# Kernel optimization log

Hardware: AMD Instinct MI355X
Metric: run time of the kernel (lower is better)

## Reference

```python
import jax, jax.numpy as jnp
import numpy as np

D_MODEL, D_STATE, B, S = 1024, 64, 8, 2048


def setup_inputs() -> dict:
    key = jax.random.key(0)
    ks = jax.random.split(key, 14)
    inp = {"x": jax.random.normal(ks[0], (B, S, D_MODEL), jnp.float32)}
    names = ["cog", "beh", "env", "delta", "Bp", "Cp"]
    for i, n in enumerate(names):
        inp[f"W_{n}"] = jax.random.normal(ks[1 + 2 * i], (D_STATE, D_MODEL), jnp.float32) / np.sqrt(D_MODEL)
        inp[f"b_{n}"] = jnp.zeros((D_STATE,), jnp.float32)
    # torch init is log(|randn|+1e-4); we use strictly-negative A_log so the
    # length-2048 multiplicative recurrence stays finite (A_log is a learned
    # parameter, so its value is free; the math of forward is unchanged).
    inp["A_log"] = -jnp.abs(jax.random.normal(ks[13], (D_STATE, D_STATE), jnp.float32)) - 0.1
    return inp


def reference(x, W_cog, b_cog, W_beh, b_beh, W_env, b_env,
              W_delta, b_delta, W_Bp, b_Bp, W_Cp, b_Cp, A_log):
    # gating terms (computed in the source but never used downstream)
    A_t = (jax.nn.sigmoid(x @ W_cog.T + b_cog)
           * jax.nn.sigmoid(x @ W_beh.T + b_beh)
           * jax.nn.sigmoid(x @ W_env.T + b_env))
    del A_t

    delta = jax.nn.softplus(x @ W_delta.T + b_delta)   # [B,S,N]
    Bt = x @ W_Bp.T + b_Bp                             # [B,S,N]
    Ct = x @ W_Cp.T + b_Cp                             # [B,S,N]
    u = Bt * x[:, :, :D_STATE]                         # [B,S,N]

    # Faithful to torch broadcasting: after step 0 the carried state h is
    # [B,N,N] with h[b,i,j] = exp(A_log[i,j]*delta[b,t,i]) * h_prev[b,i,j] + u[b,t,j]
    def step(h, td):
        d, u_t, c_t = td                               # each [B,N]
        A = jnp.exp(A_log[None, :, :] * d[:, :, None]) # [B,N,N]
        h = A * h + u_t[:, None, :]
        y = jnp.einsum('bj,bij->bi', c_t, h)           # [B,N]
        return h, y

    h0 = jnp.zeros((x.shape[0], D_STATE, D_STATE), x.dtype)
    _, ys = jax.lax.scan(
        step, h0,
        (delta.transpose(1, 0, 2), u.transpose(1, 0, 2), Ct.transpose(1, 0, 2)))
    # torch stacks y_t of shape [B,1,N] along dim=1 -> [B,S,1,N]
    return ys.transpose(1, 0, 2)[:, :, None, :]
```

## Files before the change

kernel.cpp:

```cpp
#include <hip/hip_runtime.h>
#include <math.h>

#define DM   1024
#define DS   64
#define BATCH 8
#define SEQ  2048
#define CL   32
#define NC   64

typedef __bf16 bf16x8 __attribute__((ext_vector_type(8)));
typedef float  f32x4  __attribute__((ext_vector_type(4)));

#if __has_builtin(__builtin_amdgcn_exp2f)
#define EXP2(v) __builtin_amdgcn_exp2f(v)
#else
#define EXP2(v) __expf(0.69314718056f * (v))
#endif

__global__ __launch_bounds__(256) void wconv_kernel(
    const float* __restrict__ Wd, const float* __restrict__ Wb,
    const float* __restrict__ Wc, __bf16* __restrict__ Wp)
{
    int idx = blockIdx.x * 256 + threadIdx.x;
    int k  = idx & 1023;
    int n  = idx >> 10;
    const float* W = (n < 64) ? Wd : (n < 128 ? Wb : Wc);
    float v = W[(size_t)(n & 63) * DM + k];
    int kt = k >> 5, kk = k & 31;
    Wp[((size_t)kt * 192 + n) * 32 + kk] = (__bf16)v;
}

__global__ __launch_bounds__(512, 2) void projp1_full(
    const float* __restrict__ x, const __bf16* __restrict__ Wp,
    const float* __restrict__ bd, const float* __restrict__ bb,
    const float* __restrict__ bc, const float* __restrict__ A_log,
    float* __restrict__ delta_g, float* __restrict__ u_g,
    float* __restrict__ ct_g,
    float* __restrict__ E, float* __restrict__ Dsum)
{
    __shared__ __bf16 sA[4][64 * 72];
    __shared__ float  s_d[2][CL * 64];
    __shared__ float  s_u[2][CL * 64];

    const int tid  = threadIdx.x;
    const int row0 = blockIdx.x * 64;

    const int lane = tid & 63, wv = tid >> 6;
    const int l15  = lane & 15, quad = lane >> 4;
    const int cw   = wv & 3;
    const int rh   = wv >> 2;
    const int nbase = cw * 48;
    const int rbase = rh * 32;

    const int am = tid >> 3;
    const int ak = tid & 7;
    const float* xga = x + (size_t)(row0 + am) * DM + ak * 8;

    const __bf16* wpb = Wp + (nbase + l15) * 32 + quad * 8;

    f32x4 acc[2][3];
    #pragma unroll
    for (int mt = 0; mt < 2; ++mt)
        #pragma unroll
        for (int nt = 0; nt < 3; ++nt)
            acc[mt][nt] = (f32x4){0.f, 0.f, 0.f, 0.f};

    float4 areg[4];
    bf16x8 bA[6], bB[6];

    #define LOADA2(pp) do {                                                   \
        areg[0] = *(const float4*)(xga + (pp) * 128);                         \
        areg[1] = *(const float4*)(xga + (pp) * 128 + 4);                     \
        areg[2] = *(const float4*)(xga + (pp) * 128 + 64);                    \
        areg[3] = *(const float4*)(xga + (pp) * 128 + 68);                    \
    } while (0)
    #define STAGEA2(be, bo) do {                                              \
        bf16x8 h0 = {(__bf16)areg[0].x, (__bf16)areg[0].y,                    \
                     (__bf16)areg[0].z, (__bf16)areg[0].w,                    \
                     (__bf16)areg[1].x, (__bf16)areg[1].y,                    \
                     (__bf16)areg[1].z, (__bf16)areg[1].w};                   \
        *(bf16x8*)&sA[be][am * 72 + ak * 8] = h0;                             \
        bf16x8 h1 = {(__bf16)areg[2].x, (__bf16)areg[2].y,                    \
                     (__bf16)areg[2].z, (__bf16)areg[2].w,                    \
                     (__bf16)areg[3].x, (__bf16)areg[3].y,                    \
                     (__bf16)areg[3].z, (__bf16)areg[3].w};                   \
        *(bf16x8*)&sA[bo][am * 72 + ak * 8] = h1;                             \
    } while (0)
    #define LOADBF(dst, kb) do {                                              \
        const __bf16* wb_ = wpb + (size_t)(kb) * 12288;                       \
        dst[0] = *(const bf16x8*)(wb_);                                       \
        dst[1] = *(const bf16x8*)(wb_ + 512);                                 \
        dst[2] = *(const bf16x8*)(wb_ + 1024);                                \
        dst[3] = *(const bf16x8*)(wb_ + 6144);                                \
        dst[4] = *(const bf16x8*)(wb_ + 6656);                                \
        dst[5] = *(const bf16x8*)(wb_ + 7168);                                \
    } while (0)
    #define COMPUTE(bi, bfr) do {                                             \
        _Pragma("unroll")                                                     \
        for (int s = 0; s < 2; ++s) {                                         \
            bf16x8 af0 = *(const bf16x8*)                                     \
                &sA[bi][(rbase + l15) * 72 + s * 32 + quad * 8];              \
            bf16x8 af1 = *(const bf16x8*)                                     \
                &sA[bi][(rbase + 16 + l15) * 72 + s * 32 + quad * 8];         \
            _Pragma("unroll")                                                 \
            for (int nt = 0; nt < 3; ++nt) {                                  \
                acc[0][nt] = __builtin_amdgcn_mfma_f32_16x16x32_bf16(         \
                    af0, bfr[s * 3 + nt], acc[0][nt], 0, 0, 0);               \
                acc[1][nt] = __builtin_amdgcn_mfma_f32_16x16x32_bf16(         \
                    af1, bfr[s * 3 + nt], acc[1][nt], 0, 0, 0);               \
            }                                                                 \
        }                                                                     \
    } while (0)

    LOADA2(0);
    STAGEA2(0, 1);
    LOADA2(1);
    LOADBF(bA, 0);
    __syncthreads();

    for (int p = 0; p < 8; ++p) {
        const int pe = (p & 1) * 2, po = pe + 1;
        LOADBF(bB, 2 * p + 1);
        COMPUTE(pe, bA);
        if (p < 7) STAGEA2(pe ^ 2, po ^ 2);
        if (p < 6) LOADA2(p + 2);
        if (p < 7) LOADBF(bA, 2 * p + 2);
        COMPUTE(po, bB);
        __syncthreads();
    }
    #undef LOADA2
    #undef STAGEA2
    #undef LOADBF
    #undef COMPUTE

    #pragma unroll
    for (int nt = 0; nt < 3; ++nt) {
        int gn  = nbase + nt * 16 + l15;
        int mat = (nbase + nt * 16) >> 6;
        int col = gn & 63;
        float bias = (mat == 0) ? bd[col] : (mat == 1 ? bb[col] : bc[col]);
        #pragma unroll
        for (int mt = 0; mt < 2; ++mt) {
            #pragma unroll
            for (int r = 0; r < 4; ++r) {
                int tl = mt * 16 + quad * 4 + r;
                int m  = row0 + rbase + tl;
                float v = acc[mt][nt][r] + bias;
                if (mat == 0) {
                    float sp = (v > 20.f) ? v : __logf(1.f + __expf(v));
                    delta_g[(size_t)m * DS + col] = sp;
                    s_d[rh][tl * 64 + col] = sp;
                } else if (mat == 1) {
                    float uu = v * x[(size_t)m * DM + col];
                    u_g[(size_t)m * DS + col] = uu;
                    s_u[rh][tl * 64 + col] = uu;
                } else {
                    ct_g[(size_t)m * DS + col] = v;
                }
            }
        }
    }
    __syncthreads();

    const int half = tid >> 8;
    const int bidx = blockIdx.x >> 5;
    const int cidx = (blockIdx.x * 2 + half) & 63;
    const int si = tid & 63;
    const int sj = (tid >> 6) & 3;

    float alog[16];
    {
        const float4* ar = (const float4*)(A_log + si * 64 + sj * 16);
        #pragma unroll
        for (int qq = 0; qq < 4; ++qq) {
            float4 v = ar[qq];
            alog[4*qq+0] = v.x * 1.44269504f; alog[4*qq+1] = v.y * 1.44269504f;
            alog[4*qq+2] = v.z * 1.44269504f; alog[4*qq+3] = v.w * 1.44269504f;
        }
    }

    float h[16];
    #pragma unroll
    for (int k = 0; k < 16; ++k) h[k] = 0.f;
    float dsum = 0.f;

    for (int t = 0; t < CL; ++t) {
        float d = s_d[half][t * 64 + si];
        dsum += d;
        const float* up = s_u[half] + t * 64 + sj * 16;
        #pragma unroll
        for (int k = 0; k < 16; ++k)
            h[k] = EXP2(alog[k] * d) * h[k] + up[k];
    }

    float* eo = E + (((size_t)cidx * BATCH + bidx) * 64 + si) * 64 + sj * 16;
    #pragma unroll
    for (int qq = 0; qq < 4; ++qq)
        ((float4*)eo)[qq] = make_float4(h[4*qq], h[4*qq+1], h[4*qq+2], h[4*qq+3]);
    if (sj == 0) Dsum[((size_t)cidx * BATCH + bidx) * 64 + si] = dsum;
}

__device__ __forceinline__ void scan_range8(
    const float* __restrict__ Eb, const float* __restrict__ Db,
    int n0, int n1, int bb_, int i_, int jg_,
    const float* __restrict__ alog, float* __restrict__ h)
{
    if (n0 >= n1) return;
    size_t idx = ((size_t)n0 * BATCH + bb_) * 64 + i_;
    float dsA = Db[idx];
    const float4* ep = (const float4*)(Eb + idx * 64 + jg_ * 8);
    float4 e0 = ep[0], e1 = ep[1];
    for (int n = n0; n < n1; ++n) {
        float dsN = 0.f;
        float4 f0 = make_float4(0.f,0.f,0.f,0.f), f1 = f0;
        if (n + 1 < n1) {
            size_t idx2 = ((size_t)(n + 1) * BATCH + bb_) * 64 + i_;
            dsN = Db[idx2];
            const float4* fp = (const float4*)(Eb + idx2 * 64 + jg_ * 8);
            f0 = fp[0]; f1 = fp[1];
        }
        float ev[8] = {e0.x,e0.y,e0.z,e0.w, e1.x,e1.y,e1.z,e1.w};
        #pragma unroll
        for (int k = 0; k < 8; ++k)
            h[k] = EXP2(alog[k] * dsA) * h[k] + ev[k];
        dsA = dsN; e0 = f0; e1 = f1;
    }
}

__global__ __launch_bounds__(512) void group_kernel(
    const float* __restrict__ E, const float* __restrict__ Dsum,
    const float* __restrict__ A_log,
    float* __restrict__ Eg, float* __restrict__ Dg)
{
    const int g2 = blockIdx.x >> 3, b2 = blockIdx.x & 7;
    const int tid = threadIdx.x;
    const int i  = tid >> 3;
    const int jg = tid & 7;

    float alog[8];
    {
        const float4* ar = (const float4*)(A_log + i * 64 + jg * 8);
        float4 v0 = ar[0], v1 = ar[1];
        alog[0] = v0.x * 1.44269504f; alog[1] = v0.y * 1.44269504f;
        alog[2] = v0.z * 1.44269504f; alog[3] = v0.w * 1.44269504f;
        alog[4] = v1.x * 1.44269504f; alog[5] = v1.y * 1.44269504f;
        alog[6] = v1.z * 1.44269504f; alog[7] = v1.w * 1.44269504f;
    }

    float hg[8];
    #pragma unroll
    for (int k = 0; k < 8; ++k) hg[k] = 0.f;
    scan_range8(E, Dsum, g2 * 8, g2 * 8 + 8, b2, i, jg, alog, hg);

    float4* ego = (float4*)(Eg + (((size_t)g2 * BATCH + b2) * 64 + i) * 64 + jg * 8);
    ego[0] = make_float4(hg[0], hg[1], hg[2], hg[3]);
    ego[1] = make_float4(hg[4], hg[5], hg[6], hg[7]);
    if (jg == 0) {
        float Dacc = 0.f;
        #pragma unroll
        for (int q = 0; q < 8; ++q)
            Dacc += Dsum[((size_t)(g2 * 8 + q) * BATCH + b2) * 64 + i];
        Dg[((size_t)g2 * BATCH + b2) * 64 + i] = Dacc;
    }
}

__global__ __launch_bounds__(512) void pass23_kernel(
    const float* __restrict__ delta_g, const float* __restrict__ u_g,
    const float* __restrict__ ct_g, const float* __restrict__ A_log,
    const float* __restrict__ E, const float* __restrict__ Dsum,
    const float* __restrict__ Eg, const float* __restrict__ Dg,
    float* __restrict__ out)
{
    __shared__ float s_d[CL * 64];
    __shared__ float s_u[CL * 64];
    __shared__ float s_c[CL * 64];

    const int c = blockIdx.x, b = blockIdx.y, tid = threadIdx.x;
    const int t0 = c * CL;

    {
        const float4* dg = (const float4*)(delta_g + ((size_t)b * SEQ + t0) * DS);
        const float4* ug = (const float4*)(u_g     + ((size_t)b * SEQ + t0) * DS);
        const float4* cg = (const float4*)(ct_g    + ((size_t)b * SEQ + t0) * DS);
        ((float4*)s_d)[tid] = dg[tid];
        ((float4*)s_u)[tid] = ug[tid];
        ((float4*)s_c)[tid] = cg[tid];
    }

    const int i  = tid >> 3;
    const int jg = tid & 7;

    float alog[8];
    {
        const float4* ar = (const float4*)(A_log + i * 64 + jg * 8);
        float4 v0 = ar[0], v1 = ar[1];
        alog[0] = v0.x * 1.44269504f; alog[1] = v0.y * 1.44269504f;
        alog[2] = v0.z * 1.44269504f; alog[3] = v0.w * 1.44269504f;
        alog[4] = v1.x * 1.44269504f; alog[5] = v1.y * 1.44269504f;
        alog[6] = v1.z * 1.44269504f; alog[7] = v1.w * 1.44269504f;
    }

    float h[8];
    #pragma unroll
    for (int k = 0; k < 8; ++k) h[k] = 0.f;
    const int g = c >> 3;
    scan_range8(Eg, Dg, 0, g, b, i, jg, alog, h);
    scan_range8(E, Dsum, g * 8, c, b, i, jg, alog, h);
    __syncthreads();

    for (int t = 0; t < CL; ++t) {
        float d = s_d[t * 64 + i];
        const float* up  = s_u + t * 64 + jg * 8;
        const float* cp2 = s_c + t * 64 + jg * 8;
        float part = 0.f;
        #pragma unroll
        for (int k = 0; k < 8; ++k) {
            h[k] = EXP2(alog[k] * d) * h[k] + up[k];
            part += cp2[k] * h[k];
        }
        part += __shfl_xor(part, 1);
        part += __shfl_xor(part, 2);
        part += __shfl_xor(part, 4);
        if (jg == 0)
            out[((size_t)b * SEQ + t0 + t) * DS + i] = part;
    }
}

extern "C" void kernel_launch(void* const* d_in, const int* in_sizes, int n_in,
                              void* d_out, int out_size, void* d_ws, size_t ws_size,
                              hipStream_t stream)
{
    (void)in_sizes; (void)n_in; (void)out_size; (void)ws_size;
    const float* x     = (const float*)d_in[0];
    const float* Wd    = (const float*)d_in[7];
    const float* bd    = (const float*)d_in[8];
    const float* Wb    = (const float*)d_in[9];
    const float* bb    = (const float*)d_in[10];
    const float* Wc    = (const float*)d_in[11];
    const float* bc    = (const float*)d_in[12];
    const float* A_log = (const float*)d_in[13];
    float* out = (float*)d_out;

    float* ws = (float*)d_ws;
    float* delta_g = ws;
    float* u_g     = ws + 1 * 1048576;
    float* ct_g    = ws + 2 * 1048576;
    float* E       = ws + 3 * 1048576;
    float* Dsum    = ws + 5242880;
    float* Eg      = ws + 5275648;
    float* Dg      = ws + 5537792;
    __bf16* Wp     = (__bf16*)(ws + 5541888);

    wconv_kernel<<<768, 256, 0, stream>>>(Wd, Wb, Wc, Wp);
    projp1_full<<<256, 512, 0, stream>>>(
        x, Wp, bd, bb, bc, A_log, delta_g, u_g, ct_g, E, Dsum);
    group_kernel<<<64, 512, 0, stream>>>(E, Dsum, A_log, Eg, Dg);
    pass23_kernel<<<dim3(NC, BATCH), 512, 0, stream>>>(
        delta_g, u_g, ct_g, A_log, E, Dsum, Eg, Dg, out);
}
```

Before: 170.0 us.

## Halve projection block row tile to 32 rows and double the grid

The fused projection plus chunk-scan kernel now processes 32 rows per block instead of 64, launching 512 blocks instead of 256. Each block handles one 32-step chunk, with each thread scanning 8 state columns instead of 16. Launch bounds are raised to 4 blocks per CU. The aim is more parallelism and occupancy across the CUs (256 blocks was roughly one per CU), at the cost of each block reusing the weight fragments over fewer rows and higher register pressure.

```diff
diff --git a/kernel.cpp b/kernel.cpp
--- a/kernel.cpp
+++ b/kernel.cpp
@@ -30,7 +30,7 @@
     Wp[((size_t)kt * 192 + n) * 32 + kk] = (__bf16)v;
 }
 
-__global__ __launch_bounds__(512, 2) void projp1_full(
+__global__ __launch_bounds__(512, 4) void projp1_full(
     const float* __restrict__ x, const __bf16* __restrict__ Wp,
     const float* __restrict__ bd, const float* __restrict__ bb,
     const float* __restrict__ bc, const float* __restrict__ A_log,
@@ -38,53 +38,46 @@
     float* __restrict__ ct_g,
     float* __restrict__ E, float* __restrict__ Dsum)
 {
-    __shared__ __bf16 sA[4][64 * 72];
-    __shared__ float  s_d[2][CL * 64];
-    __shared__ float  s_u[2][CL * 64];
+    __shared__ __bf16 sA[4][32 * 72];
+    __shared__ float  s_d[CL * 64];
+    __shared__ float  s_u[CL * 64];
 
     const int tid  = threadIdx.x;
-    const int row0 = blockIdx.x * 64;
+    const int row0 = blockIdx.x * 32;
 
     const int lane = tid & 63, wv = tid >> 6;
     const int l15  = lane & 15, quad = lane >> 4;
     const int cw   = wv & 3;
     const int rh   = wv >> 2;
     const int nbase = cw * 48;
-    const int rbase = rh * 32;
-
-    const int am = tid >> 3;
-    const int ak = tid & 7;
-    const float* xga = x + (size_t)(row0 + am) * DM + ak * 8;
+    const int rbase = rh * 16;
+
+    const int am    = tid >> 4;
+    const int aslot = tid & 15;
+    const int asub  = aslot >> 3;
+    const int aoff  = (aslot & 7) * 8;
+    const float* xga = x + (size_t)(row0 + am) * DM + aslot * 8;
 
     const __bf16* wpb = Wp + (nbase + l15) * 32 + quad * 8;
 
-    f32x4 acc[2][3];
-    #pragma unroll
-    for (int mt = 0; mt < 2; ++mt)
-        #pragma unroll
-        for (int nt = 0; nt < 3; ++nt)
-            acc[mt][nt] = (f32x4){0.f, 0.f, 0.f, 0.f};
-
-    float4 areg[4];
+    f32x4 acc[3];
+    #pragma unroll
+    for (int nt = 0; nt < 3; ++nt)
+        acc[nt] = (f32x4){0.f, 0.f, 0.f, 0.f};
+
+    float4 areg[2];
     bf16x8 bA[6], bB[6];
 
     #define LOADA2(pp) do {                                                   \
         areg[0] = *(const float4*)(xga + (pp) * 128);                         \
         areg[1] = *(const float4*)(xga + (pp) * 128 + 4);                     \
-        areg[2] = *(const float4*)(xga + (pp) * 128 + 64);                    \
-        areg[3] = *(const float4*)(xga + (pp) * 128 + 68);                    \
     } while (0)
-    #define STAGEA2(be, bo) do {                                              \
-        bf16x8 h0 = {(__bf16)areg[0].x, (__bf16)areg[0].y,                    \
+    #define STAGEA2(be) do {                                                  \
+        bf16x8 hv = {(__bf16)areg[0].x, (__bf16)areg[0].y,                    \
                      (__bf16)areg[0].z, (__bf16)areg[0].w,                    \
                      (__bf16)areg[1].x, (__bf16)areg[1].y,                    \
                      (__bf16)areg[1].z, (__bf16)areg[1].w};                   \
-        *(bf16x8*)&sA[be][am * 72 + ak * 8] = h0;                             \
-        bf16x8 h1 = {(__bf16)areg[2].x, (__bf16)areg[2].y,                    \
-                     (__bf16)areg[2].z, (__bf16)areg[2].w,                    \
-                     (__bf16)areg[3].x, (__bf16)areg[3].y,                    \
-                     (__bf16)areg[3].z, (__bf16)areg[3].w};                   \
-        *(bf16x8*)&sA[bo][am * 72 + ak * 8] = h1;                             \
+        *(bf16x8*)&sA[(be) + asub][am * 72 + aoff] = hv;                      \
     } while (0)
     #define LOADBF(dst, kb) do {                                              \
         const __bf16* wb_ = wpb + (size_t)(kb) * 12288;                       \
@@ -98,22 +91,17 @@
     #define COMPUTE(bi, bfr) do {                                             \
         _Pragma("unroll")                                                     \
         for (int s = 0; s < 2; ++s) {                                         \
-            bf16x8 af0 = *(const bf16x8*)                                     \
+            bf16x8 af = *(const bf16x8*)                                      \
                 &sA[bi][(rbase + l15) * 72 + s * 32 + quad * 8];              \
-            bf16x8 af1 = *(const bf16x8*)                                     \
-                &sA[bi][(rbase + 16 + l15) * 72 + s * 32 + quad * 8];         \
             _Pragma("unroll")                                                 \
-            for (int nt = 0; nt < 3; ++nt) {                                  \
-                acc[0][nt] = __builtin_amdgcn_mfma_f32_16x16x32_bf16(         \
-                    af0, bfr[s * 3 + nt], acc[0][nt], 0, 0, 0);               \
-                acc[1][nt] = __builtin_amdgcn_mfma_f32_16x16x32_bf16(         \
-                    af1, bfr[s * 3 + nt], acc[1][nt], 0, 0, 0);               \
-            }                                                                 \
+            for (int nt = 0; nt < 3; ++nt)                                    \
+                acc[nt] = __builtin_amdgcn_mfma_f32_16x16x32_bf16(            \
+                    af, bfr[s * 3 + nt], acc[nt], 0, 0, 0);                   \
         }                                                                     \
     } while (0)
 
     LOADA2(0);
-    STAGEA2(0, 1);
+    STAGEA2(0);
     LOADA2(1);
     LOADBF(bA, 0);
     __syncthreads();
@@ -122,7 +110,7 @@
         const int pe = (p & 1) * 2, po = pe + 1;
         LOADBF(bB, 2 * p + 1);
         COMPUTE(pe, bA);
-        if (p < 7) STAGEA2(pe ^ 2, po ^ 2);
+        if (p < 7) STAGEA2(pe ^ 2);
         if (p < 6) LOADA2(p + 2);
         if (p < 7) LOADBF(bA, 2 * p + 2);
         COMPUTE(po, bB);
@@ -140,64 +128,58 @@
         int col = gn & 63;
         float bias = (mat == 0) ? bd[col] : (mat == 1 ? bb[col] : bc[col]);
         #pragma unroll
-        for (int mt = 0; mt < 2; ++mt) {
-            #pragma unroll
-            for (int r = 0; r < 4; ++r) {
-                int tl = mt * 16 + quad * 4 + r;
-                int m  = row0 + rbase + tl;
-                float v = acc[mt][nt][r] + bias;
-                if (mat == 0) {
-                    float sp = (v > 20.f) ? v : __logf(1.f + __expf(v));
-                    delta_g[(size_t)m * DS + col] = sp;
-                    s_d[rh][tl * 64 + col] = sp;
-                } else if (mat == 1) {
-                    float uu = v * x[(size_t)m * DM + col];
-                    u_g[(size_t)m * DS + col] = uu;
-                    s_u[rh][tl * 64 + col] = uu;
-                } else {
-                    ct_g[(size_t)m * DS + col] = v;
-                }
+        for (int r = 0; r < 4; ++r) {
+            int tl = rbase + quad * 4 + r;
+            int m  = row0 + tl;
+            float v = acc[nt][r] + bias;
+            if (mat == 0) {
+                float sp = (v > 20.f) ? v : __logf(1.f + __expf(v));
+                delta_g[(size_t)m * DS + col] = sp;
+                s_d[tl * 64 + col] = sp;
+            } else if (mat == 1) {
+                float uu = v * x[(size_t)m * DM + col];
+                u_g[(size_t)m * DS + col] = uu;
+                s_u[tl * 64 + col] = uu;
+            } else {
+                ct_g[(size_t)m * DS + col] = v;
             }
         }
     }
     __syncthreads();
 
-    const int half = tid >> 8;
-    const int bidx = blockIdx.x >> 5;
-    const int cidx = (blockIdx.x * 2 + half) & 63;
-    const int si = tid & 63;
-    const int sj = (tid >> 6) & 3;
-
-    float alog[16];
+    const int bidx = blockIdx.x >> 6;
+    const int cidx = blockIdx.x & 63;
+    const int i  = tid >> 3;
+    const int jg = tid & 7;
+
+    float alog[8];
     {
-        const float4* ar = (const float4*)(A_log + si * 64 + sj * 16);
-        #pragma unroll
-        for (int qq = 0; qq < 4; ++qq) {
-            float4 v = ar[qq];
-            alog[4*qq+0] = v.x * 1.44269504f; alog[4*qq+1] = v.y * 1.44269504f;
-            alog[4*qq+2] = v.z * 1.44269504f; alog[4*qq+3] = v.w * 1.44269504f;
-        }
-    }
-
-    float h[16];
-    #pragma unroll
-    for (int k = 0; k < 16; ++k) h[k] = 0.f;
+        const float4* ar = (const float4*)(A_log + i * 64 + jg * 8);
+        float4 v0 = ar[0], v1 = ar[1];
+        alog[0] = v0.x * 1.44269504f; alog[1] = v0.y * 1.44269504f;
+        alog[2] = v0.z * 1.44269504f; alog[3] = v0.w * 1.44269504f;
+        alog[4] = v1.x * 1.44269504f; alog[5] = v1.y * 1.44269504f;
+        alog[6] = v1.z * 1.44269504f; alog[7] = v1.w * 1.44269504f;
+    }
+
+    float h[8];
+    #pragma unroll
+    for (int k = 0; k < 8; ++k) h[k] = 0.f;
     float dsum = 0.f;
 
     for (int t = 0; t < CL; ++t) {
-        float d = s_d[half][t * 64 + si];
+        float d = s_d[t * 64 + i];
         dsum += d;
-        const float* up = s_u[half] + t * 64 + sj * 16;
-        #pragma unroll
-        for (int k = 0; k < 16; ++k)
+        const float* up = s_u + t * 64 + jg * 8;
+        #pragma unroll
+        for (int k = 0; k < 8; ++k)
             h[k] = EXP2(alog[k] * d) * h[k] + up[k];
     }
 
-    float* eo = E + (((size_t)cidx * BATCH + bidx) * 64 + si) * 64 + sj * 16;
-    #pragma unroll
-    for (int qq = 0; qq < 4; ++qq)
-        ((float4*)eo)[qq] = make_float4(h[4*qq], h[4*qq+1], h[4*qq+2], h[4*qq+3]);
-    if (sj == 0) Dsum[((size_t)cidx * BATCH + bidx) * 64 + si] = dsum;
+    float* eo = E + (((size_t)cidx * BATCH + bidx) * 64 + i) * 64 + jg * 8;
+    ((float4*)eo)[0] = make_float4(h[0], h[1], h[2], h[3]);
+    ((float4*)eo)[1] = make_float4(h[4], h[5], h[6], h[7]);
+    if (jg == 0) Dsum[((size_t)cidx * BATCH + bidx) * 64 + i] = dsum;
 }
 
 __device__ __forceinline__ void scan_range8(
@@ -352,7 +334,7 @@
     __bf16* Wp     = (__bf16*)(ws + 5541888);
 
     wconv_kernel<<<768, 256, 0, stream>>>(Wd, Wb, Wc, Wp);
-    projp1_full<<<256, 512, 0, stream>>>(
+    projp1_full<<<512, 512, 0, stream>>>(
         x, Wp, bd, bb, bc, A_log, delta_g, u_g, ct_g, E, Dsum);
     group_kernel<<<64, 512, 0, stream>>>(E, Dsum, A_log, Eg, Dg);
     pass23_kernel<<<dim3(NC, BATCH), 512, 0, stream>>>(
```

Result: slower. 178.6 us (+5.0%).

## Shrink projection blocks to 32 rows and use lightweight LDS-only barriers

Applied to the files above, without the earlier changes.

The fused projection plus chunk-scan kernel now runs 512 blocks of 256 threads, each handling one 32-row chunk instead of two, and the shared-memory buffers shrink to match. Every wave now owns all 32 rows for a 48-column slice, so each block's weight loads are shared by fewer rows. __syncthreads is replaced by a barrier that waits only on LDS counters and not on outstanding global loads, so prefetches can stay in flight across the barrier. This trades more total weight traffic and block count for finer-grained scheduling and smaller per-block LDS.

```diff
diff --git a/kernel.cpp b/kernel.cpp
--- a/kernel.cpp
+++ b/kernel.cpp
@@ -16,6 +16,12 @@
 #else
 #define EXP2(v) __expf(0.69314718056f * (v))
 #endif
+
+#define LBAR() do {                                                           \
+    asm volatile("s_waitcnt lgkmcnt(0)" ::: "memory");                        \
+    __builtin_amdgcn_s_barrier();                                             \
+    asm volatile("" ::: "memory");                                            \
+} while (0)
 
 __global__ __launch_bounds__(256) void wconv_kernel(
     const float* __restrict__ Wd, const float* __restrict__ Wb,
@@ -30,7 +36,7 @@
     Wp[((size_t)kt * 192 + n) * 32 + kk] = (__bf16)v;
 }
 
-__global__ __launch_bounds__(512, 2) void projp1_full(
+__global__ __launch_bounds__(256, 2) void projp1_full(
     const float* __restrict__ x, const __bf16* __restrict__ Wp,
     const float* __restrict__ bd, const float* __restrict__ bb,
     const float* __restrict__ bc, const float* __restrict__ A_log,
@@ -38,19 +44,16 @@
     float* __restrict__ ct_g,
     float* __restrict__ E, float* __restrict__ Dsum)
 {
-    __shared__ __bf16 sA[4][64 * 72];
-    __shared__ float  s_d[2][CL * 64];
-    __shared__ float  s_u[2][CL * 64];
+    __shared__ __bf16 sA[4][32 * 72];
+    __shared__ float  s_d[CL * 64];
+    __shared__ float  s_u[CL * 64];
 
     const int tid  = threadIdx.x;
-    const int row0 = blockIdx.x * 64;
+    const int row0 = blockIdx.x * 32;
 
     const int lane = tid & 63, wv = tid >> 6;
     const int l15  = lane & 15, quad = lane >> 4;
-    const int cw   = wv & 3;
-    const int rh   = wv >> 2;
-    const int nbase = cw * 48;
-    const int rbase = rh * 32;
+    const int nbase = wv * 48;
 
     const int am = tid >> 3;
     const int ak = tid & 7;
@@ -99,9 +102,9 @@
         _Pragma("unroll")                                                     \
         for (int s = 0; s < 2; ++s) {                                         \
             bf16x8 af0 = *(const bf16x8*)                                     \
-                &sA[bi][(rbase + l15) * 72 + s * 32 + quad * 8];              \
+                &sA[bi][(l15) * 72 + s * 32 + quad * 8];                      \
             bf16x8 af1 = *(const bf16x8*)                                     \
-                &sA[bi][(rbase + 16 + l15) * 72 + s * 32 + quad * 8];         \
+                &sA[bi][(16 + l15) * 72 + s * 32 + quad * 8];                 \
             _Pragma("unroll")                                                 \
             for (int nt = 0; nt < 3; ++nt) {                                  \
                 acc[0][nt] = __builtin_amdgcn_mfma_f32_16x16x32_bf16(         \
@@ -116,7 +119,7 @@
     STAGEA2(0, 1);
     LOADA2(1);
     LOADBF(bA, 0);
-    __syncthreads();
+    LBAR();
 
     for (int p = 0; p < 8; ++p) {
         const int pe = (p & 1) * 2, po = pe + 1;
@@ -126,7 +129,7 @@
         if (p < 6) LOADA2(p + 2);
         if (p < 7) LOADBF(bA, 2 * p + 2);
         COMPUTE(po, bB);
-        __syncthreads();
+        LBAR();
     }
     #undef LOADA2
     #undef STAGEA2
@@ -144,29 +147,28 @@
             #pragma unroll
             for (int r = 0; r < 4; ++r) {
                 int tl = mt * 16 + quad * 4 + r;
-                int m  = row0 + rbase + tl;
+                int m  = row0 + tl;
                 float v = acc[mt][nt][r] + bias;
                 if (mat == 0) {
                     float sp = (v > 20.f) ? v : __logf(1.f + __expf(v));
                     delta_g[(size_t)m * DS + col] = sp;
-                    s_d[rh][tl * 64 + col] = sp;
+                    s_d[tl * 64 + col] = sp;
                 } else if (mat == 1) {
                     float uu = v * x[(size_t)m * DM + col];
                     u_g[(size_t)m * DS + col] = uu;
-                    s_u[rh][tl * 64 + col] = uu;
+                    s_u[tl * 64 + col] = uu;
                 } else {
                     ct_g[(size_t)m * DS + col] = v;
                 }
             }
         }
     }
-    __syncthreads();
-
-    const int half = tid >> 8;
-    const int bidx = blockIdx.x >> 5;
-    const int cidx = (blockIdx.x * 2 + half) & 63;
+    LBAR();
+
+    const int bidx = row0 >> 11;
+    const int cidx = (row0 >> 5) & 63;
     const int si = tid & 63;
-    const int sj = (tid >> 6) & 3;
+    const int sj = tid >> 6;
 
     float alog[16];
     {
@@ -185,9 +187,9 @@
     float dsum = 0.f;
 
     for (int t = 0; t < CL; ++t) {
-        float d = s_d[half][t * 64 + si];
+        float d = s_d[t * 64 + si];
         dsum += d;
-        const float* up = s_u[half] + t * 64 + sj * 16;
+        const float* up = s_u + t * 64 + sj * 16;
         #pragma unroll
         for (int k = 0; k < 16; ++k)
             h[k] = EXP2(alog[k] * d) * h[k] + up[k];
@@ -352,7 +354,7 @@
     __bf16* Wp     = (__bf16*)(ws + 5541888);
 
     wconv_kernel<<<768, 256, 0, stream>>>(Wd, Wb, Wc, Wp);
-    projp1_full<<<256, 512, 0, stream>>>(
+    projp1_full<<<512, 256, 0, stream>>>(
         x, Wp, bd, bb, bc, A_log, delta_g, u_g, ct_g, E, Dsum);
     group_kernel<<<64, 512, 0, stream>>>(E, Dsum, A_log, Eg, Dg);
     pass23_kernel<<<dim3(NC, BATCH), 512, 0, stream>>>(
```

Result: no change. 170.7 us (+0.4%).
